# Optimization experiments

Measured on AMD Instinct MI355X. Metric: run time of the kernel, lower is better.

Reference implementation:

```python
import jax, jax.numpy as jnp
import numpy as np

KERNEL = 3          # kernel_size = (3, 3)
DEGREE = 3          # spline_order -> Chebyshev polynomial degree
N_CONVS = 8


def setup_inputs() -> dict:
    key = jax.random.key(0)
    k1, k2, k3, k4 = jax.random.split(key, 4)
    x = jax.random.normal(k1, (16, 16, 128, 128), jnp.float32)
    # per-conv learned params of ChebyshevKANLinear(in=9, out=1), stacked over n_convs
    cheby_coeffs = jax.random.normal(k2, (N_CONVS, KERNEL * KERNEL, DEGREE + 1), jnp.float32) * 0.1
    base_weight = jax.random.normal(k3, (N_CONVS, KERNEL * KERNEL), jnp.float32) * (1.0 / 3.0)
    spline_scaler = 1.0 + 0.1 * jax.random.normal(k4, (N_CONVS, KERNEL * KERNEL), jnp.float32)
    return {"x": x, "cheby_coeffs": cheby_coeffs,
            "base_weight": base_weight, "spline_scaler": spline_scaler}


def _kan_conv2d(x, cheby_coeffs, base_weight, spline_scaler):
    # x: (B, C, H, W); each channel unfolded independently (as torch Unfold per-channel),
    # each of N_CONVS KAN kernels applied to every channel -> out channels C*N_CONVS.
    B, C, H, W = x.shape
    patches = jax.lax.conv_general_dilated_patches(
        x, (KERNEL, KERNEL), (1, 1), [(1, 1), (1, 1)])  # (B, C*9, Ho, Wo), channel-major
    Ho, Wo = patches.shape[-2], patches.shape[-1]
    p = patches.reshape(B, C, KERNEL * KERNEL, Ho * Wo)
    p = jnp.moveaxis(p, 2, 3)  # (B, C, P, 9) where P = Ho*Wo patches

    # base (skip) path: SiLU(x) @ base_weight^T
    base = jnp.einsum('bcpi,ji->bcjp', jax.nn.silu(p), base_weight)

    # spline path: Chebyshev basis on tanh-normalized input
    t = jnp.tanh(p)
    Ts = [jnp.ones_like(t), t]
    for _ in range(DEGREE - 1):
        Ts.append(2.0 * t * Ts[-1] - Ts[-2])
    Tb = jnp.stack(Ts, axis=-1)  # (B, C, P, 9, DEGREE+1)
    w = cheby_coeffs * spline_scaler[..., None]  # (n_convs, 9, D+1)
    spline = jnp.einsum('bcpik,jik->bcjp', Tb, w)

    out = (base + spline).reshape(B, C * N_CONVS, Ho, Wo)
    return out


def reference(x, cheby_coeffs, base_weight, spline_scaler):
    return _kan_conv2d(x, cheby_coeffs, base_weight, spline_scaler)
```

## Files before the change

### kernel.cpp

```cpp
#include <hip/hip_runtime.h>

#define BATCH 16
#define CH    16
#define HH    128
#define WW    128
#define NC    8
#define TR    8
#define BPB   4
#define HR    (TR + 2)
#define FW    (WW + 2)
#define NELEM (HR * FW)
#define NSTG  ((NELEM + 255) / 256)

__global__ __launch_bounds__(256, 4)
void kan_conv_kernel(const float* __restrict__ x,
                     const float* __restrict__ cheby,
                     const float* __restrict__ bwt,
                     const float* __restrict__ scl,
                     float* __restrict__ out)
{
    __shared__ float4 feat[HR][FW];
    __shared__ float4 wgt[9 * NC];
    __shared__ float  bias[NC];

    const int tid   = threadIdx.x;
    const int bz    = blockIdx.y;
    const int band0 = blockIdx.x * (TR * BPB);

    const float* xp = x + (size_t)bz * HH * WW;

    if (tid < 9 * NC) {
        int j = tid / 9, i = tid % 9;
        float s = scl[j * 9 + i];
        wgt[i * NC + j] = make_float4(bwt[j * 9 + i],
                                      cheby[(j * 9 + i) * 4 + 1] * s,
                                      cheby[(j * 9 + i) * 4 + 2] * s,
                                      cheby[(j * 9 + i) * 4 + 3] * s);
    } else if (tid >= 128 && tid < 128 + NC) {
        int j = tid - 128;
        float b = 0.f;
        #pragma unroll
        for (int i = 0; i < 9; ++i)
            b += (cheby[(j * 9 + i) * 4 + 0] - cheby[(j * 9 + i) * 4 + 2]) * scl[j * 9 + i];
        bias[j] = b;
    }

    int srow[NSTG], scol[NSTG];
    #pragma unroll
    for (int k = 0; k < NSTG; ++k) {
        int idx = tid + 256 * k;
        srow[k] = idx / FW;
        scol[k] = idx - srow[k] * FW;
    }

    float v[NSTG];
    #pragma unroll
    for (int k = 0; k < NSTG; ++k) {
        int idx = tid + 256 * k;
        int gh  = band0 + srow[k] - 1;
        int gw  = scol[k] - 1;
        float nv = 0.f;
        if (idx < NELEM && (unsigned)gh < (unsigned)HH && (unsigned)gw < (unsigned)WW)
            nv = xp[gh * WW + gw];
        v[k] = nv;
    }

    for (int bb = 0; bb < BPB; ++bb) {
        const int band = band0 + bb * TR;

        #pragma unroll
        for (int k = 0; k < NSTG; ++k) {
            int idx = tid + 256 * k;
            if (idx < NELEM) {
                float val = v[k];
                float e1 = __expf(val);
                float e2 = e1 * e1;
                float sg = 1.f - __builtin_amdgcn_rcpf(1.f + e1);
                float t  = 1.f - 2.f * __builtin_amdgcn_rcpf(e2 + 1.f);
                float f2 = 2.f * t * t;
                float f3 = 2.f * t * (f2 - 1.f) - t;
                feat[srow[k]][scol[k]] = make_float4(val * sg, t, f2, f3);
            }
        }
        __syncthreads();

        if (bb + 1 < BPB) {
            const int nb = band + TR;
            #pragma unroll
            for (int k = 0; k < NSTG; ++k) {
                int idx = tid + 256 * k;
                int gh  = nb + srow[k] - 1;
                int gw  = scol[k] - 1;
                float nv = 0.f;
                if (idx < NELEM && (unsigned)gh < (unsigned)HH && (unsigned)gw < (unsigned)WW)
                    nv = xp[gh * WW + gw];
                v[k] = nv;
            }
        }

        const int c  = tid & 127;
        const int r0 = tid >> 7;

        float acc[4][NC];
        #pragma unroll
        for (int s = 0; s < 4; ++s)
            #pragma unroll
            for (int j = 0; j < NC; ++j)
                acc[s][j] = bias[j];

        #pragma unroll
        for (int dr = 0; dr < 3; ++dr) {
            #pragma unroll
            for (int dc = 0; dc < 3; ++dc) {
                float4 f[4];
                #pragma unroll
                for (int s = 0; s < 4; ++s)
                    f[s] = feat[r0 + 2 * s + dr][c + dc];
                #pragma unroll
                for (int j = 0; j < NC; ++j) {
                    float4 w = wgt[(dr * 3 + dc) * NC + j];
                    #pragma unroll
                    for (int s = 0; s < 4; ++s) {
                        acc[s][j] += w.x * f[s].x;
                        acc[s][j] += w.y * f[s].y;
                        acc[s][j] += w.z * f[s].z;
                        acc[s][j] += w.w * f[s].w;
                    }
                }
            }
        }

        float* op = out + (size_t)(bz * NC) * HH * WW + (size_t)(band + r0) * WW + c;
        #pragma unroll
        for (int j = 0; j < NC; ++j)
            #pragma unroll
            for (int s = 0; s < 4; ++s)
                op[(size_t)j * HH * WW + s * 2 * WW] = acc[s][j];

        __syncthreads();
    }
}

extern "C" void kernel_launch(void* const* d_in, const int* in_sizes, int n_in,
                              void* d_out, int out_size, void* d_ws, size_t ws_size,
                              hipStream_t stream) {
    const float* x     = (const float*)d_in[0];
    const float* cheby = (const float*)d_in[1];
    const float* bwt   = (const float*)d_in[2];
    const float* scl   = (const float*)d_in[3];
    float* out = (float*)d_out;

    dim3 grid(HH / (TR * BPB), BATCH * CH);
    dim3 block(256);
    hipLaunchKernelGGL(kan_conv_kernel, grid, block, 0, stream, x, cheby, bwt, scl, out);
}
```

Before: 159.3 us.

## Precompute folded KAN weights in a prep kernel and read them from global memory

Adds a small prep kernel that folds spline scalers into the Chebyshev coefficients and computes the constant bias once, writing them to the workspace. The main kernel then reads weights directly from global memory (uniform, likely scalar loads) instead of rebuilding LDS copies in every block. It also recomputes staging row/column indices instead of keeping them in registers, halves bands per block to double the grid, and raises the occupancy hint from 4 to 5. The cost is an extra kernel launch, weight loads through global memory in the inner loop, and reloading the halo for more blocks.

```diff
diff --git a/kernel.cpp b/kernel.cpp
--- a/kernel.cpp
+++ b/kernel.cpp
@@ -6,59 +6,59 @@
 #define WW    128
 #define NC    8
 #define TR    8
-#define BPB   4
+#define BPB   2
 #define HR    (TR + 2)
 #define FW    (WW + 2)
 #define NELEM (HR * FW)
 #define NSTG  ((NELEM + 255) / 256)
 
-__global__ __launch_bounds__(256, 4)
+__global__ void prep_weights(const float* __restrict__ cheby,
+                             const float* __restrict__ bwt,
+                             const float* __restrict__ scl,
+                             float* __restrict__ ws)
+{
+    const int tid = threadIdx.x;
+    if (tid < 72) {
+        int i = tid >> 3;
+        int j = tid & 7;
+        float s = scl[j * 9 + i];
+        ((float4*)ws)[tid] = make_float4(bwt[j * 9 + i],
+                                         cheby[(j * 9 + i) * 4 + 1] * s,
+                                         cheby[(j * 9 + i) * 4 + 2] * s,
+                                         cheby[(j * 9 + i) * 4 + 3] * s);
+    } else if (tid < 80) {
+        int j = tid - 72;
+        float b = 0.f;
+        #pragma unroll
+        for (int i = 0; i < 9; ++i)
+            b += (cheby[(j * 9 + i) * 4 + 0] - cheby[(j * 9 + i) * 4 + 2]) * scl[j * 9 + i];
+        ws[288 + j] = b;
+    }
+}
+
+__global__ __launch_bounds__(256, 5)
 void kan_conv_kernel(const float* __restrict__ x,
-                     const float* __restrict__ cheby,
-                     const float* __restrict__ bwt,
-                     const float* __restrict__ scl,
+                     const float* __restrict__ wb,
                      float* __restrict__ out)
 {
     __shared__ float4 feat[HR][FW];
-    __shared__ float4 wgt[9 * NC];
-    __shared__ float  bias[NC];
 
     const int tid   = threadIdx.x;
     const int bz    = blockIdx.y;
     const int band0 = blockIdx.x * (TR * BPB);
 
     const float* xp = x + (size_t)bz * HH * WW;
-
-    if (tid < 9 * NC) {
-        int j = tid / 9, i = tid % 9;
-        float s = scl[j * 9 + i];
-        wgt[i * NC + j] = make_float4(bwt[j * 9 + i],
-                                      cheby[(j * 9 + i) * 4 + 1] * s,
-                                      cheby[(j * 9 + i) * 4 + 2] * s,
-                                      cheby[(j * 9 + i) * 4 + 3] * s);
-    } else if (tid >= 128 && tid < 128 + NC) {
-        int j = tid - 128;
-        float b = 0.f;
-        #pragma unroll
-        for (int i = 0; i < 9; ++i)
-            b += (cheby[(j * 9 + i) * 4 + 0] - cheby[(j * 9 + i) * 4 + 2]) * scl[j * 9 + i];
-        bias[j] = b;
-    }
-
-    int srow[NSTG], scol[NSTG];
-    #pragma unroll
-    for (int k = 0; k < NSTG; ++k) {
-        int idx = tid + 256 * k;
-        srow[k] = idx / FW;
-        scol[k] = idx - srow[k] * FW;
-    }
+    const float4* __restrict__ wq = (const float4*)wb;
+    const float*  __restrict__ bp = wb + 288;
 
     float v[NSTG];
     #pragma unroll
     for (int k = 0; k < NSTG; ++k) {
         int idx = tid + 256 * k;
-        int gh  = band0 + srow[k] - 1;
-        int gw  = scol[k] - 1;
+        int row = idx / FW;
+        int col = idx - row * FW;
+        int gh  = band0 + row - 1;
+        int gw  = col - 1;
         float nv = 0.f;
         if (idx < NELEM && (unsigned)gh < (unsigned)HH && (unsigned)gw < (unsigned)WW)
             nv = xp[gh * WW + gw];
@@ -72,6 +72,8 @@
         for (int k = 0; k < NSTG; ++k) {
             int idx = tid + 256 * k;
             if (idx < NELEM) {
+                int row = idx / FW;
+                int col = idx - row * FW;
                 float val = v[k];
                 float e1 = __expf(val);
                 float e2 = e1 * e1;
@@ -79,7 +81,7 @@
                 float t  = 1.f - 2.f * __builtin_amdgcn_rcpf(e2 + 1.f);
                 float f2 = 2.f * t * t;
                 float f3 = 2.f * t * (f2 - 1.f) - t;
-                feat[srow[k]][scol[k]] = make_float4(val * sg, t, f2, f3);
+                feat[row][col] = make_float4(val * sg, t, f2, f3);
             }
         }
         __syncthreads();
@@ -89,8 +91,10 @@
             #pragma unroll
             for (int k = 0; k < NSTG; ++k) {
                 int idx = tid + 256 * k;
-                int gh  = nb + srow[k] - 1;
-                int gw  = scol[k] - 1;
+                int row = idx / FW;
+                int col = idx - row * FW;
+                int gh  = nb + row - 1;
+                int gw  = col - 1;
                 float nv = 0.f;
                 if (idx < NELEM && (unsigned)gh < (unsigned)HH && (unsigned)gw < (unsigned)WW)
                     nv = xp[gh * WW + gw];
@@ -106,7 +110,7 @@
         for (int s = 0; s < 4; ++s)
             #pragma unroll
             for (int j = 0; j < NC; ++j)
-                acc[s][j] = bias[j];
+                acc[s][j] = bp[j];
 
         #pragma unroll
         for (int dr = 0; dr < 3; ++dr) {
@@ -118,7 +122,7 @@
                     f[s] = feat[r0 + 2 * s + dr][c + dc];
                 #pragma unroll
                 for (int j = 0; j < NC; ++j) {
-                    float4 w = wgt[(dr * 3 + dc) * NC + j];
+                    float4 w = wq[(dr * 3 + dc) * NC + j];
                     #pragma unroll
                     for (int s = 0; s < 4; ++s) {
                         acc[s][j] += w.x * f[s].x;
@@ -149,8 +153,12 @@
     const float* bwt   = (const float*)d_in[2];
     const float* scl   = (const float*)d_in[3];
     float* out = (float*)d_out;
+    float* ws  = (float*)d_ws;
+
+    hipLaunchKernelGGL(prep_weights, dim3(1), dim3(128), 0, stream,
+                       cheby, bwt, scl, ws);
 
     dim3 grid(HH / (TR * BPB), BATCH * CH);
     dim3 block(256);
-    hipLaunchKernelGGL(kan_conv_kernel, grid, block, 0, stream, x, cheby, bwt, scl, out);
+    hipLaunchKernelGGL(kan_conv_kernel, grid, block, 0, stream, x, ws, out);
 }
```

Measured after the change: 190.3 us. 1.19x slower.
